# Kernel tuning notes

Hardware: AMD Instinct MI355X
Metric: run time of the kernel (lower is better)

Reference implementation:

```python
import jax, jax.numpy as jnp
import numpy as np

B, T, S, O = 8, 60, 36, 1
H, E, PE = 4, 16, 16
AD, TA, OUT, L = 12, 10, 64, 2
PRUNE_KEEP_FROM = int(np.floor(S * S * 0.5))  # floor(S^2 * (1 - prune_rate))
EPS = 1e-5


def lrelu(v):
    return jax.nn.leaky_relu(v, 0.01)


def pos_encode(times):
    # standard sinusoidal PE on raw timestamps -> (B, T, PE)
    half = PE // 2
    div = jnp.exp(jnp.arange(half, dtype=jnp.float32) * (-jnp.log(10000.0) / half))
    ang = times[..., None] * div
    return jnp.stack([jnp.sin(ang), jnp.cos(ang)], axis=-1).reshape(times.shape + (PE,))


def pair_sim(adj):
    # sum_{i<j} ||a_i - a_j||^2 = B*sum_i||a_i||^2 - ||sum_i a_i||^2
    b = adj.shape[0]
    sq = jnp.sum(adj * adj)
    tot = jnp.sum(adj, axis=0)
    return (b * sq - jnp.sum(tot * tot)) / ((b - 1) ** 2) / (S * S)


def _forward(x, times, mask, bn_g, bn_b, obs_emb_w, attn_w, bidir_w, proj_W, proj_b,
             Wq, bq, Wk, bk, Ws, bs, lnt_g, lnt_b, Wse, bse, lns_g, lns_b):
    b = x.shape[0]
    # BatchNorm2d over timestep channels (training-mode batch stats)
    mu = x.mean(axis=(0, 2, 3), keepdims=True)
    var = x.var(axis=(0, 2, 3), keepdims=True)
    x = (x - mu) / jnp.sqrt(var + EPS) * bn_g[None, :, None, None] + bn_b[None, :, None, None]
    # per-sensor observation embedding: (B,T,S,O) x (S,O,E*H) -> (B,H,T,S,E)
    h = lrelu(jnp.einsum('btso,som->btsm', x, obs_emb_w))
    h = h.reshape(b, T, S, H, E).transpose(0, 3, 1, 2, 4)
    h = h * mask[:, None, :, :, None]
    pe = pos_encode(times)  # (B,T,PE)
    adj = jnp.ones((b, H, S, S), x.dtype)
    sim = pair_sim(adj)  # 0 for all-ones init, kept for faithfulness
    prune_msk = None
    for lay in range(L):
        hp = h @ proj_W.T + proj_b  # (B,H,T,S,AD+PE)
        cat = jnp.concatenate([
            jnp.broadcast_to(attn_w[lay][None, :, None], (b, H, T, S, AD)),
            jnp.broadcast_to(pe[:, None, :, None], (b, H, T, S, PE))], axis=-1)
        alpha = lrelu(jnp.einsum('bhtsd,bhtjd->bhtsj', hp, cat))  # (B,H,T,S,S)
        if lay:
            cnt = mask.sum(axis=1)[:, None, :, None]  # (B,1,S,1)
            adj = lrelu(adj * (alpha.sum(axis=2) / cnt))
            if prune_msk is None:
                flat = adj.reshape(b, H, S * S)
                ranks = jnp.argsort(jnp.argsort(flat, axis=-1), axis=-1)
                prune_msk = (ranks >= PRUNE_KEEP_FROM).astype(adj.dtype).reshape(b, H, S, S)
            adj = adj * prune_msk
            sim = sim + pair_sim(adj)
        bidir = lrelu(jnp.einsum('hsd,hjd->hsj', bidir_w[lay], bidir_w[lay]))  # (H,S,S)
        w = lrelu(bidir[None, :, None] * alpha * adj[:, :, None])  # (B,H,T,S,S)
        # broadcast message passing: (B,H,T,1,S,E) * (B,H,T,S,S,1) -> sum over source sensor
        h = lrelu(jnp.sum(lrelu(h[:, :, :, None, :, :] * w[..., None]), axis=4))
    pe_e = jnp.broadcast_to(pe[:, None, :, None], (b, H, T, S, PE))
    Hc = jnp.concatenate([h, pe_e], axis=-1).transpose(0, 1, 3, 2, 4)  # (B,H,S,T,E+PE)
    Q = Hc @ Wq.T + bq
    K = Hc @ Wk.T + bk
    beta = jnp.einsum('bhstd,bhsud->bhstu', Q, K)  # (B,H,S,T,T)
    beta = (beta @ Ws.T + bs)[..., 0]  # (B,H,S,T)
    m = beta.mean(axis=(-2, -1), keepdims=True)
    v = beta.var(axis=(-2, -1), keepdims=True)
    beta = (beta - m) / jnp.sqrt(v + EPS) * lnt_g + lnt_b
    out = lrelu(jnp.einsum('bhst,bhstd->bhsd', beta, Hc))
    out = lrelu(out @ Wse.T + bse)
    m2 = out.mean(axis=(-2, -1), keepdims=True)
    v2 = out.var(axis=(-2, -1), keepdims=True)
    out = (out - m2) / jnp.sqrt(v2 + EPS) * lns_g + lns_b
    out = out.transpose(0, 2, 1, 3).reshape(b, S, OUT)
    return out, sim


def setup_inputs():
    key = jax.random.key(0)
    ks = jax.random.split(key, 12)
    def rn(k, shape, scale=0.1):
        return jax.random.normal(k, shape, jnp.float32) * scale
    return {
        'x': jax.random.normal(ks[0], (B, T, S, O), jnp.float32),
        'times': jnp.tile(jnp.arange(T, dtype=jnp.float32), (B, 1)),
        'mask': jnp.ones((B, T, S), jnp.float32),
        'bn_g': jnp.ones((T,), jnp.float32),
        'bn_b': jnp.zeros((T,), jnp.float32),
        'obs_emb_w': rn(ks[1], (S, O, E * H)),
        'attn_w': rn(ks[2], (L, H, S, AD)),
        'bidir_w': rn(ks[3], (L, H, S, AD)),
        'proj_W': rn(ks[4], (AD + PE, E)),
        'proj_b': jnp.zeros((AD + PE,), jnp.float32),
        'Wq': rn(ks[5], (TA, E + PE)),
        'bq': jnp.zeros((TA,), jnp.float32),
        'Wk': rn(ks[6], (TA, E + PE)),
        'bk': jnp.zeros((TA,), jnp.float32),
        'Ws': rn(ks[7], (1, T)),
        'bs': jnp.zeros((1,), jnp.float32),
        'lnt_g': jnp.ones((S, T), jnp.float32),
        'lnt_b': jnp.zeros((S, T), jnp.float32),
        'Wse': rn(ks[8], (OUT // H, E + PE)),
        'bse': jnp.zeros((OUT // H,), jnp.float32),
        'lns_g': jnp.ones((S, OUT // H), jnp.float32),
        'lns_b': jnp.zeros((S, OUT // H), jnp.float32),
    }


def reference(x, times, mask, bn_g, bn_b, obs_emb_w, attn_w, bidir_w, proj_W, proj_b,
              Wq, bq, Wk, bk, Ws, bs, lnt_g, lnt_b, Wse, bse, lns_g, lns_b):
    return _forward(x, times, mask, bn_g, bn_b, obs_emb_w, attn_w, bidir_w, proj_W, proj_b,
                    Wq, bq, Wk, bk, Ws, bs, lnt_g, lnt_b, Wse, bse, lns_g, lns_b)
```

## Files before the change

kernel.cpp:

```cpp
#include <hip/hip_runtime.h>
#include <math.h>

#define Bc 8
#define Tc 60
#define Sc 36
#define Hc_ 4
#define Ec 16
#define PEc 16
#define ADc 12
#define TAc 10
#define OUTc 64
#define KEEP 648
#define EPSc 1e-5f
#define LOG1E4_8 1.15129254649702284f

#define WS_H2     18176
#define WS_H1     1124096
#define WS_ALPHA  2230016
#define WS_ADJ    4759808
#define WS_ADJP   4801280
#define WS_CNT    5050112
#define WS_BETA   WS_ALPHA
#define WS_PART   (WS_ALPHA + 69120)
#define WS_OUT2   (WS_ALPHA + 71424)
#define WS_PART2  (WS_ALPHA + 89856)

__device__ __forceinline__ float lrelu(float v){ return v >= 0.f ? v : 0.01f*v; }

__global__ __launch_bounds__(256) void k_layer01(const float* __restrict__ x,
                          const float* __restrict__ times,
                          const float* __restrict__ mask,
                          const float* __restrict__ bn_g,
                          const float* __restrict__ bn_b,
                          const float* __restrict__ obs_w,
                          const float* __restrict__ attn,
                          const float* __restrict__ bidw,
                          const float* __restrict__ projW,
                          const float* __restrict__ projb,
                          float* __restrict__ ws){
    int idx = blockIdx.x;
    int t = idx % Tc; int bh = idx / Tc; int h = bh % Hc_; int b = bh / Hc_;
    int tid = threadIdx.x;
    __shared__ float sh_h[Sc*Ec];
    __shared__ float sh_h1[Sc*Ec];
    __shared__ float sh_pe[PEc];
    __shared__ float sh_at0T[ADc*Sc];
    __shared__ float sh_at1T[ADc*Sc];
    __shared__ float sh_bwT[ADc*Sc];
    __shared__ float sh_hp[Sc*28];
    __shared__ float sh_P[Sc];
    __shared__ float sh_w[Sc*Sc];
    __shared__ float sh_xn[Sc];
    __shared__ float sh_m[Sc];
    __shared__ float sred[8];
    float s0 = 0.f, s1 = 0.f;
    for (int i = tid; i < Bc*Sc; i += 256){
        float v = x[((i/Sc)*Tc + t)*Sc + (i%Sc)];
        s0 += v; s1 += v*v;
    }
    #pragma unroll
    for (int off = 32; off; off >>= 1){
        s0 += __shfl_down(s0, off, 64);
        s1 += __shfl_down(s1, off, 64);
    }
    if ((tid & 63) == 0){ sred[(tid>>6)*2] = s0; sred[(tid>>6)*2 + 1] = s1; }
    if (tid >= 64 && tid < 80){
        int q = tid - 64; int j = q >> 1;
        float ang = times[b*Tc + t] * expf(-(float)j * LOG1E4_8);
        sh_pe[q] = (q & 1) ? cosf(ang) : sinf(ang);
    }
    for (int i = tid; i < ADc*Sc; i += 256){
        int d = i / Sc, j = i % Sc;
        sh_at0T[i] = attn[h*Sc*ADc + j*ADc + d];
        sh_at1T[i] = attn[(Hc_ + h)*Sc*ADc + j*ADc + d];
        sh_bwT[i]  = bidw[h*Sc*ADc + j*ADc + d];
    }
    __syncthreads();
    float mu  = (sred[0]+sred[2]+sred[4]+sred[6]) / (float)(Bc*Sc);
    float var = (sred[1]+sred[3]+sred[5]+sred[7]) / (float)(Bc*Sc) - mu*mu;
    if (tid < Sc){
        float xv = x[(b*Tc + t)*Sc + tid];
        sh_xn[tid] = (xv - mu) * rsqrtf(var + EPSc) * bn_g[t] + bn_b[t];
        sh_m[tid]  = mask[(b*Tc + t)*Sc + tid];
    }
    __syncthreads();
    for (int i = tid; i < Sc*Ec; i += 256){
        int s = i / Ec, e = i % Ec;
        sh_h[i] = lrelu(sh_xn[s]*obs_w[s*64 + h*Ec + e]) * sh_m[s];
    }
    __syncthreads();
    for (int i = tid; i < Sc*28; i += 256){
        int s = i / 28, d = i % 28;
        float acc = projb[d];
        const float* w = projW + d*Ec;
        const float* hh = sh_h + s*Ec;
        #pragma unroll
        for (int e = 0; e < Ec; e++) acc += hh[e]*w[e];
        sh_hp[i] = acc;
    }
    __syncthreads();
    if (tid < Sc){
        const float* hp = sh_hp + tid*28 + ADc;
        float p = 0.f;
        #pragma unroll
        for (int d = 0; d < PEc; d++) p += hp[d]*sh_pe[d];
        sh_P[tid] = p;
    }
    __syncthreads();
    for (int i = tid; i < Sc*Sc; i += 256){
        int s = i / Sc, j = i % Sc;
        const float* hp = sh_hp + s*28;
        float acc = sh_P[s];
        float bd = 0.f;
        #pragma unroll
        for (int d = 0; d < ADc; d++){
            acc += hp[d]*sh_at0T[d*Sc + j];
            bd  += sh_bwT[d*Sc + s]*sh_bwT[d*Sc + j];
        }
        sh_w[i] = lrelu(lrelu(bd)*lrelu(acc));
    }
    __syncthreads();
    float* h1g = ws + WS_H1 + (size_t)idx*Sc*Ec;
    for (int i = tid; i < Sc*Ec; i += 256){
        int s = i / Ec, e = i % Ec;
        float acc = 0.f;
        #pragma unroll 6
        for (int j = 0; j < Sc; j++) acc += lrelu(sh_h[j*Ec + e]*sh_w[s*Sc + j]);
        float v = lrelu(acc);
        sh_h1[i] = v;
        h1g[i] = v;
    }
    __syncthreads();
    for (int i = tid; i < Sc*28; i += 256){
        int s = i / 28, d = i % 28;
        float acc = projb[d];
        const float* w = projW + d*Ec;
        const float* hh = sh_h1 + s*Ec;
        #pragma unroll
        for (int e = 0; e < Ec; e++) acc += hh[e]*w[e];
        sh_hp[i] = acc;
    }
    __syncthreads();
    if (tid < Sc){
        const float* hp = sh_hp + tid*28 + ADc;
        float p = 0.f;
        #pragma unroll
        for (int d = 0; d < PEc; d++) p += hp[d]*sh_pe[d];
        sh_P[tid] = p;
    }
    __syncthreads();
    float* adst = ws + WS_ALPHA + (size_t)idx*Sc*Sc;
    for (int i = tid; i < Sc*Sc; i += 256){
        int s = i / Sc, j = i % Sc;
        const float* hp = sh_hp + s*28;
        float acc = sh_P[s];
        #pragma unroll
        for (int d = 0; d < ADc; d++) acc += hp[d]*sh_at1T[d*Sc + j];
        adst[i] = lrelu(acc);
    }
}

__global__ __launch_bounds__(256) void k_adjpart(const float* __restrict__ mask, float* __restrict__ ws){
    int bh = blockIdx.x / 6; int chunk = blockIdx.x % 6;
    int tid = threadIdx.x;
    const float4* a = (const float4*)(ws + WS_ALPHA + (size_t)bh*Tc*Sc*Sc) + (size_t)chunk*10*324;
    float4* p = (float4*)(ws + WS_ADJP + (size_t)blockIdx.x*Sc*Sc);
    for (int c = tid; c < 324; c += 256){
        float4 acc = make_float4(0.f, 0.f, 0.f, 0.f);
        #pragma unroll
        for (int tt = 0; tt < 10; tt++){
            float4 u = a[(size_t)tt*324 + c];
            acc.x += u.x; acc.y += u.y; acc.z += u.z; acc.w += u.w;
        }
        p[c] = acc;
    }
    if (chunk == 0 && (bh & 3) == 0 && tid < Sc){
        int b = bh >> 2;
        float c = 0.f;
        #pragma unroll 4
        for (int t = 0; t < Tc; t++) c += mask[(b*Tc + t)*Sc + tid];
        ws[WS_CNT + b*Sc + tid] = c;
    }
}

__global__ __launch_bounds__(256) void k_prune(float* __restrict__ ws){
    int bh = blockIdx.x / 24; int chunk = blockIdx.x % 24;
    int b = bh >> 2;
    int tid = threadIdx.x;
    __shared__ __align__(16) float sh_v[Sc*Sc];
    __shared__ float sh_cnt[Sc];
    const float4* p = (const float4*)(ws + WS_ADJP + (size_t)bh*6*Sc*Sc);
    for (int c = tid; c < 324; c += 256){
        float4 acc = make_float4(0.f, 0.f, 0.f, 0.f);
        #pragma unroll
        for (int q = 0; q < 6; q++){
            float4 u = p[(size_t)q*324 + c];
            acc.x += u.x; acc.y += u.y; acc.z += u.z; acc.w += u.w;
        }
        ((float4*)sh_v)[c] = acc;
    }
    if (tid < Sc) sh_cnt[tid] = ws[WS_CNT + b*Sc + tid];
    __syncthreads();
    for (int i = tid; i < Sc*Sc; i += 256){
        int s = i / Sc;
        sh_v[i] = lrelu(sh_v[i] / sh_cnt[s]);
    }
    __syncthreads();
    int r = tid >> 2; if (r > 53) r = 53;
    int part = tid & 3;
    int i = chunk*54 + r;
    float v = sh_v[i];
    const float4* v4 = (const float4*)sh_v + part*81;
    int a0 = part*324;
    int cnt = 0;
    #pragma unroll 9
    for (int j = 0; j < 81; j++){
        float4 u = v4[j];
        int k = a0 + j*4;
        cnt += (int)(u.x < v) + ((int)(u.x == v) & (int)(k   < i));
        cnt += (int)(u.y < v) + ((int)(u.y == v) & (int)(k+1 < i));
        cnt += (int)(u.z < v) + ((int)(u.z == v) & (int)(k+2 < i));
        cnt += (int)(u.w < v) + ((int)(u.w == v) & (int)(k+3 < i));
    }
    cnt += __shfl_down(cnt, 2, 4);
    cnt += __shfl_down(cnt, 1, 4);
    if (part == 0 && tid < 216)
        ws[WS_ADJ + bh*Sc*Sc + i] = (cnt >= KEEP) ? v : 0.f;
}

__global__ __launch_bounds__(256) void k_layer1mp(const float* __restrict__ bidw,
                                                  float* __restrict__ ws){
    int idx = blockIdx.x;
    int bh = idx / Tc; int h = bh % Hc_;
    int tid = threadIdx.x;
    __shared__ float sh_h[Sc*Ec];
    __shared__ float sh_w[Sc*Sc];
    __shared__ float sh_bwT[ADc*Sc];
    const float* hsrc = ws + WS_H1 + (size_t)idx*Sc*Ec;
    float*       hdst = ws + WS_H2 + (size_t)idx*Sc*Ec;
    const float* al  = ws + WS_ALPHA + (size_t)idx*Sc*Sc;
    const float* adj = ws + WS_ADJ + bh*Sc*Sc;
    for (int i = tid; i < Sc*Ec; i += 256) sh_h[i] = hsrc[i];
    for (int i = tid; i < ADc*Sc; i += 256){
        int d = i / Sc, j = i % Sc;
        sh_bwT[i] = bidw[(Hc_ + h)*Sc*ADc + j*ADc + d];
    }
    __syncthreads();
    for (int i = tid; i < Sc*Sc; i += 256){
        int s = i / Sc, j = i % Sc;
        float bd = 0.f;
        #pragma unroll
        for (int d = 0; d < ADc; d++) bd += sh_bwT[d*Sc + s]*sh_bwT[d*Sc + j];
        sh_w[i] = lrelu(lrelu(bd)*al[i]*adj[i]);
    }
    __syncthreads();
    for (int i = tid; i < Sc*Ec; i += 256){
        int s = i / Ec, e = i % Ec;
        float acc = 0.f;
        #pragma unroll 6
        for (int j = 0; j < Sc; j++) acc += lrelu(sh_h[j*Ec + e]*sh_w[s*Sc + j]);
        hdst[i] = lrelu(acc);
    }
}

__global__ __launch_bounds__(64) void kF1(const float* __restrict__ Wq, const float* __restrict__ bq,
                   const float* __restrict__ Wk, const float* __restrict__ bk,
                   const float* __restrict__ Ws_, const float* __restrict__ bs_,
                   const float* __restrict__ times, float* __restrict__ ws){
    int idx = blockIdx.x;
    int s = idx % Sc; int bh = idx / Sc; int b = bh / Hc_;
    int tid = threadIdx.x;
    __shared__ float sh_Hc[Tc*33];
    __shared__ float sh_K[Tc*11];
    __shared__ float sh_Wq[TAc*32];
    __shared__ float sh_WkT[32*TAc];
    __shared__ float sh_bq[TAc], sh_bk[TAc];
    __shared__ float sh_ws[Tc];
    __shared__ float sh_Kw[TAc];
    const float* h2 = ws + WS_H2 + (size_t)bh*Tc*Sc*Ec + s*Ec;
    for (int i4 = tid; i4 < Tc*4; i4 += 64){
        int t = i4 >> 2, c4 = i4 & 3;
        float4 u = *(const float4*)(h2 + t*Sc*Ec + c4*4);
        float* d = sh_Hc + t*33 + c4*4;
        d[0] = u.x; d[1] = u.y; d[2] = u.z; d[3] = u.w;
    }
    for (int i = tid; i < Tc*PEc; i += 64){
        int t = i / PEc, q = i % PEc; int j = q >> 1;
        float ang = times[b*Tc + t] * expf(-(float)j * LOG1E4_8);
        sh_Hc[t*33 + Ec + q] = (q & 1) ? cosf(ang) : sinf(ang);
    }
    for (int i = tid; i < TAc*32; i += 64){
        sh_Wq[i] = Wq[i];
        int d = i / 32, q = i % 32;
        sh_WkT[q*TAc + d] = Wk[i];
    }
    if (tid < TAc){ sh_bq[tid] = bq[tid]; sh_bk[tid] = bk[tid]; }
    if (tid < Tc) sh_ws[tid] = Ws_[tid];
    __syncthreads();
    for (int i = tid; i < Tc*TAc; i += 64){
        int t = i / TAc, d = i % TAc;
        const float* hc = sh_Hc + t*33;
        float acc = sh_bk[d];
        #pragma unroll
        for (int q = 0; q < 32; q++) acc += hc[q]*sh_WkT[q*TAc + d];
        sh_K[t*11 + d] = acc;
    }
    __syncthreads();
    if (tid < TAc){
        float acc = 0.f;
        #pragma unroll 4
        for (int t = 0; t < Tc; t++) acc += sh_K[t*11 + tid]*sh_ws[t];
        sh_Kw[tid] = acc;
    }
    __syncthreads();
    float bv = 0.f;
    float bsv = bs_[0];
    if (tid < Tc){
        const float* hc = sh_Hc + tid*33;
        float acc = bsv;
        #pragma unroll
        for (int d = 0; d < TAc; d++){
            const float* wq = sh_Wq + d*32;
            float qv = sh_bq[d];
            #pragma unroll
            for (int q = 0; q < 32; q++) qv += hc[q]*wq[q];
            acc += qv*sh_Kw[d];
        }
        bv = acc;
        ws[WS_BETA + idx*Tc + tid] = acc;
    }
    float p0 = (tid < Tc) ? bv : 0.f;
    float p1 = p0*bv;
    #pragma unroll
    for (int off = 32; off; off >>= 1){
        p0 += __shfl_down(p0, off, 64);
        p1 += __shfl_down(p1, off, 64);
    }
    if (tid == 0){
        ws[WS_PART + idx*2]     = p0;
        ws[WS_PART + idx*2 + 1] = p1;
    }
}

__global__ __launch_bounds__(64) void kF2(const float* __restrict__ lnt_g, const float* __restrict__ lnt_b,
                   const float* __restrict__ Wse, const float* __restrict__ bse,
                   const float* __restrict__ times, float* __restrict__ ws){
    int idx = blockIdx.x;
    int s = idx % Sc; int bh = idx / Sc; int b = bh / Hc_;
    int tid = threadIdx.x;
    __shared__ float sh_Hc[Tc*33];
    __shared__ float sh_beta[Tc];
    __shared__ float sh_o1[32];
    __shared__ float sh_mi[2];
    float p0 = 0.f, p1 = 0.f;
    if (tid < Sc){
        p0 = ws[WS_PART + (bh*Sc + tid)*2];
        p1 = ws[WS_PART + (bh*Sc + tid)*2 + 1];
    }
    #pragma unroll
    for (int off = 32; off; off >>= 1){
        p0 += __shfl_down(p0, off, 64);
        p1 += __shfl_down(p1, off, 64);
    }
    if (tid == 0){
        float m = p0 / (float)(Sc*Tc);
        sh_mi[0] = m;
        sh_mi[1] = rsqrtf(p1 / (float)(Sc*Tc) - m*m + EPSc);
    }
    const float* h2 = ws + WS_H2 + (size_t)bh*Tc*Sc*Ec + s*Ec;
    for (int i4 = tid; i4 < Tc*4; i4 += 64){
        int t = i4 >> 2, c4 = i4 & 3;
        float4 u = *(const float4*)(h2 + t*Sc*Ec + c4*4);
        float* d = sh_Hc + t*33 + c4*4;
        d[0] = u.x; d[1] = u.y; d[2] = u.z; d[3] = u.w;
    }
    for (int i = tid; i < Tc*PEc; i += 64){
        int t = i / PEc, q = i % PEc; int j = q >> 1;
        float ang = times[b*Tc + t] * expf(-(float)j * LOG1E4_8);
        sh_Hc[t*33 + Ec + q] = (q & 1) ? cosf(ang) : sinf(ang);
    }
    __syncthreads();
    float m = sh_mi[0], inv = sh_mi[1];
    if (tid < Tc){
        float bvv = ws[WS_BETA + idx*Tc + tid];
        sh_beta[tid] = (bvv - m)*inv*lnt_g[s*Tc + tid] + lnt_b[s*Tc + tid];
    }
    __syncthreads();
    if (tid < 32){
        float acc = 0.f;
        #pragma unroll 4
        for (int t = 0; t < Tc; t++) acc += sh_beta[t]*sh_Hc[t*33 + tid];
        sh_o1[tid] = lrelu(acc);
    }
    __syncthreads();
    float v = 0.f;
    if (tid < 16){
        float acc = bse[tid];
        const float* w = Wse + tid*32;
        #pragma unroll
        for (int d = 0; d < 32; d++) acc += sh_o1[d]*w[d];
        v = lrelu(acc);
        ws[WS_OUT2 + idx*16 + tid] = v;
    }
    float q0 = v, q1 = v*v;
    #pragma unroll
    for (int off = 32; off; off >>= 1){
        q0 += __shfl_down(q0, off, 64);
        q1 += __shfl_down(q1, off, 64);
    }
    if (tid == 0){
        ws[WS_PART2 + idx*2]     = q0;
        ws[WS_PART2 + idx*2 + 1] = q1;
    }
}

__global__ __launch_bounds__(256) void kF3s(const float* __restrict__ lns_g, const float* __restrict__ lns_b,
                    const float* __restrict__ ws, float* __restrict__ out){
    int tid = threadIdx.x;
    if (blockIdx.x == 32){
        float sq = 0.f, t2 = 0.f;
        for (int i = tid; i < Hc_*Sc*Sc; i += 256){
            float tot = 0.f;
            #pragma unroll
            for (int b = 0; b < Bc; b++){
                float v = ws[WS_ADJ + b*Hc_*Sc*Sc + i];
                sq += v*v; tot += v;
            }
            t2 += tot*tot;
        }
        __shared__ float r0[256], r1[256];
        r0[tid] = sq; r1[tid] = t2; __syncthreads();
        for (int off = 128; off; off >>= 1){
            if (tid < off){ r0[tid] += r0[tid+off]; r1[tid] += r1[tid+off]; }
            __syncthreads();
        }
        if (tid == 0)
            out[Bc*Sc*OUTc] = ((float)Bc*r0[0] - r1[0]) / 49.f / 1296.f;
        return;
    }
    int bh = blockIdx.x; int h = bh % Hc_; int b = bh / Hc_;
    __shared__ float sh_mi[2];
    if (tid < 64){
        float p0 = 0.f, p1 = 0.f;
        if (tid < Sc){
            p0 = ws[WS_PART2 + (bh*Sc + tid)*2];
            p1 = ws[WS_PART2 + (bh*Sc + tid)*2 + 1];
        }
        #pragma unroll
        for (int off = 32; off; off >>= 1){
            p0 += __shfl_down(p0, off, 64);
            p1 += __shfl_down(p1, off, 64);
        }
        if (tid == 0){
            float m = p0 / (float)(Sc*16);
            sh_mi[0] = m;
            sh_mi[1] = rsqrtf(p1 / (float)(Sc*16) - m*m + EPSc);
        }
    }
    __syncthreads();
    float m2 = sh_mi[0], inv2 = sh_mi[1];
    for (int i = tid; i < Sc*16; i += 256){
        int s = i / 16, k = i % 16;
        float v = ws[WS_OUT2 + bh*Sc*16 + i];
        out[(b*Sc + s)*OUTc + h*16 + k] = (v - m2)*inv2*lns_g[i] + lns_b[i];
    }
}

extern "C" void kernel_launch(void* const* d_in, const int* in_sizes, int n_in,
                              void* d_out, int out_size, void* d_ws, size_t ws_size,
                              hipStream_t stream){
    const float* x     = (const float*)d_in[0];
    const float* times = (const float*)d_in[1];
    const float* mask  = (const float*)d_in[2];
    const float* bn_g  = (const float*)d_in[3];
    const float* bn_b  = (const float*)d_in[4];
    const float* obs   = (const float*)d_in[5];
    const float* attn  = (const float*)d_in[6];
    const float* bidw  = (const float*)d_in[7];
    const float* projW = (const float*)d_in[8];
    const float* projb = (const float*)d_in[9];
    const float* Wq    = (const float*)d_in[10];
    const float* bq    = (const float*)d_in[11];
    const float* Wk    = (const float*)d_in[12];
    const float* bk    = (const float*)d_in[13];
    const float* Ws_   = (const float*)d_in[14];
    const float* bs_   = (const float*)d_in[15];
    const float* lnt_g = (const float*)d_in[16];
    const float* lnt_b = (const float*)d_in[17];
    const float* Wse   = (const float*)d_in[18];
    const float* bse   = (const float*)d_in[19];
    const float* lns_g = (const float*)d_in[20];
    const float* lns_b = (const float*)d_in[21];
    float* ws  = (float*)d_ws;
    float* out = (float*)d_out;

    k_layer01<<<Bc*Hc_*Tc, 256, 0, stream>>>(x, times, mask, bn_g, bn_b, obs, attn, bidw, projW, projb, ws);
    k_adjpart<<<Bc*Hc_*6, 256, 0, stream>>>(mask, ws);
    k_prune<<<Bc*Hc_*24, 256, 0, stream>>>(ws);
    k_layer1mp<<<Bc*Hc_*Tc, 256, 0, stream>>>(bidw, ws);
    kF1<<<Bc*Hc_*Sc, 64, 0, stream>>>(Wq, bq, Wk, bk, Ws_, bs_, times, ws);
    kF2<<<Bc*Hc_*Sc, 64, 0, stream>>>(lnt_g, lnt_b, Wse, bse, times, ws);
    kF3s<<<Bc*Hc_ + 1, 256, 0, stream>>>(lns_g, lns_b, ws, out);
}
```

Before: 209.8 us.

## Precompute bidir weights and positional encodings, fold final layernorm into kF2 via tickets

Computes the layer-1 bidirectional weight matrix and the sinusoidal positional encodings once per (b,h) and per b inside k_adjpart and stores them in workspace, so k_layer1mp, kF1 and kF2 no longer recompute them per block. The adjacency-similarity reduction moves into an extra block of k_layer1mp. The last kF2 block per (b,h), chosen with an atomic ticket counter, applies the final layernorm, which removes the kF3s launch. This trades redundant math and one kernel launch for extra workspace traffic plus threadfence and atomic synchronization.

```diff
diff --git a/kernel.cpp b/kernel.cpp
--- a/kernel.cpp
+++ b/kernel.cpp
@@ -20,6 +20,9 @@
 #define WS_ADJ    4759808
 #define WS_ADJP   4801280
 #define WS_CNT    5050112
+#define WS_BID1   5050400
+#define WS_PET    5091872
+#define WS_TKT    5099552
 #define WS_BETA   WS_ALPHA
 #define WS_PART   (WS_ALPHA + 69120)
 #define WS_OUT2   (WS_ALPHA + 71424)
@@ -160,7 +163,10 @@
     }
 }
 
-__global__ __launch_bounds__(256) void k_adjpart(const float* __restrict__ mask, float* __restrict__ ws){
+__global__ __launch_bounds__(256) void k_adjpart(const float* __restrict__ mask,
+                          const float* __restrict__ bidw,
+                          const float* __restrict__ times,
+                          float* __restrict__ ws){
     int bh = blockIdx.x / 6; int chunk = blockIdx.x % 6;
     int tid = threadIdx.x;
     const float4* a = (const float4*)(ws + WS_ALPHA + (size_t)bh*Tc*Sc*Sc) + (size_t)chunk*10*324;
@@ -180,6 +186,27 @@
         #pragma unroll 4
         for (int t = 0; t < Tc; t++) c += mask[(b*Tc + t)*Sc + tid];
         ws[WS_CNT + b*Sc + tid] = c;
+    }
+    if (blockIdx.x == 0 && tid < 32)
+        ((int*)(ws + WS_TKT))[tid] = 0;
+    if (chunk == 1){
+        int h = bh % Hc_;
+        const float* bw = bidw + (Hc_ + h)*Sc*ADc;
+        for (int i = tid; i < Sc*Sc; i += 256){
+            int s = i / Sc, j = i % Sc;
+            float bd = 0.f;
+            #pragma unroll
+            for (int d = 0; d < ADc; d++) bd += bw[s*ADc + d]*bw[j*ADc + d];
+            ws[WS_BID1 + bh*Sc*Sc + i] = lrelu(bd);
+        }
+    }
+    if (chunk == 2 && (bh & 3) == 0){
+        int b = bh >> 2;
+        for (int i = tid; i < Tc*PEc; i += 256){
+            int t = i / PEc, q = i % PEc; int j = q >> 1;
+            float ang = times[b*Tc + t] * expf(-(float)j * LOG1E4_8);
+            ws[WS_PET + (b*Tc + t)*PEc + q] = (q & 1) ? cosf(ang) : sinf(ang);
+        }
     }
 }
 
@@ -228,31 +255,41 @@
         ws[WS_ADJ + bh*Sc*Sc + i] = (cnt >= KEEP) ? v : 0.f;
 }
 
-__global__ __launch_bounds__(256) void k_layer1mp(const float* __restrict__ bidw,
-                                                  float* __restrict__ ws){
+__global__ __launch_bounds__(256) void k_layer1mp(float* __restrict__ ws, float* __restrict__ out){
+    int tid = threadIdx.x;
+    if (blockIdx.x == Bc*Hc_*Tc){
+        float sq = 0.f, t2 = 0.f;
+        for (int i = tid; i < Hc_*Sc*Sc; i += 256){
+            float tot = 0.f;
+            #pragma unroll
+            for (int b = 0; b < Bc; b++){
+                float v = ws[WS_ADJ + b*Hc_*Sc*Sc + i];
+                sq += v*v; tot += v;
+            }
+            t2 += tot*tot;
+        }
+        __shared__ float r0[256], r1[256];
+        r0[tid] = sq; r1[tid] = t2; __syncthreads();
+        for (int off = 128; off; off >>= 1){
+            if (tid < off){ r0[tid] += r0[tid+off]; r1[tid] += r1[tid+off]; }
+            __syncthreads();
+        }
+        if (tid == 0)
+            out[Bc*Sc*OUTc] = ((float)Bc*r0[0] - r1[0]) / 49.f / 1296.f;
+        return;
+    }
     int idx = blockIdx.x;
-    int bh = idx / Tc; int h = bh % Hc_;
-    int tid = threadIdx.x;
+    int bh = idx / Tc;
     __shared__ float sh_h[Sc*Ec];
     __shared__ float sh_w[Sc*Sc];
-    __shared__ float sh_bwT[ADc*Sc];
     const float* hsrc = ws + WS_H1 + (size_t)idx*Sc*Ec;
     float*       hdst = ws + WS_H2 + (size_t)idx*Sc*Ec;
     const float* al  = ws + WS_ALPHA + (size_t)idx*Sc*Sc;
     const float* adj = ws + WS_ADJ + bh*Sc*Sc;
+    const float* bid = ws + WS_BID1 + bh*Sc*Sc;
     for (int i = tid; i < Sc*Ec; i += 256) sh_h[i] = hsrc[i];
-    for (int i = tid; i < ADc*Sc; i += 256){
-        int d = i / Sc, j = i % Sc;
-        sh_bwT[i] = bidw[(Hc_ + h)*Sc*ADc + j*ADc + d];
-    }
-    __syncthreads();
-    for (int i = tid; i < Sc*Sc; i += 256){
-        int s = i / Sc, j = i % Sc;
-        float bd = 0.f;
-        #pragma unroll
-        for (int d = 0; d < ADc; d++) bd += sh_bwT[d*Sc + s]*sh_bwT[d*Sc + j];
-        sh_w[i] = lrelu(lrelu(bd)*al[i]*adj[i]);
-    }
+    for (int i = tid; i < Sc*Sc; i += 256)
+        sh_w[i] = lrelu(bid[i]*al[i]*adj[i]);
     __syncthreads();
     for (int i = tid; i < Sc*Ec; i += 256){
         int s = i / Ec, e = i % Ec;
@@ -266,7 +303,7 @@
 __global__ __launch_bounds__(64) void kF1(const float* __restrict__ Wq, const float* __restrict__ bq,
                    const float* __restrict__ Wk, const float* __restrict__ bk,
                    const float* __restrict__ Ws_, const float* __restrict__ bs_,
-                   const float* __restrict__ times, float* __restrict__ ws){
+                   float* __restrict__ ws){
     int idx = blockIdx.x;
     int s = idx % Sc; int bh = idx / Sc; int b = bh / Hc_;
     int tid = threadIdx.x;
@@ -284,11 +321,9 @@
         float* d = sh_Hc + t*33 + c4*4;
         d[0] = u.x; d[1] = u.y; d[2] = u.z; d[3] = u.w;
     }
-    for (int i = tid; i < Tc*PEc; i += 64){
-        int t = i / PEc, q = i % PEc; int j = q >> 1;
-        float ang = times[b*Tc + t] * expf(-(float)j * LOG1E4_8);
-        sh_Hc[t*33 + Ec + q] = (q & 1) ? cosf(ang) : sinf(ang);
-    }
+    const float* pet = ws + WS_PET + b*Tc*PEc;
+    for (int i = tid; i < Tc*PEc; i += 64)
+        sh_Hc[(i/PEc)*33 + Ec + (i%PEc)] = pet[i];
     for (int i = tid; i < TAc*32; i += 64){
         sh_Wq[i] = Wq[i];
         int d = i / 32, q = i % 32;
@@ -344,14 +379,16 @@
 
 __global__ __launch_bounds__(64) void kF2(const float* __restrict__ lnt_g, const float* __restrict__ lnt_b,
                    const float* __restrict__ Wse, const float* __restrict__ bse,
-                   const float* __restrict__ times, float* __restrict__ ws){
+                   const float* __restrict__ lns_g, const float* __restrict__ lns_b,
+                   float* __restrict__ ws, float* __restrict__ out){
     int idx = blockIdx.x;
-    int s = idx % Sc; int bh = idx / Sc; int b = bh / Hc_;
+    int s = idx % Sc; int bh = idx / Sc; int b = bh / Hc_; int h = bh % Hc_;
     int tid = threadIdx.x;
     __shared__ float sh_Hc[Tc*33];
     __shared__ float sh_beta[Tc];
     __shared__ float sh_o1[32];
     __shared__ float sh_mi[2];
+    __shared__ int sh_last;
     float p0 = 0.f, p1 = 0.f;
     if (tid < Sc){
         p0 = ws[WS_PART + (bh*Sc + tid)*2];
@@ -374,11 +411,9 @@
         float* d = sh_Hc + t*33 + c4*4;
         d[0] = u.x; d[1] = u.y; d[2] = u.z; d[3] = u.w;
     }
-    for (int i = tid; i < Tc*PEc; i += 64){
-        int t = i / PEc, q = i % PEc; int j = q >> 1;
-        float ang = times[b*Tc + t] * expf(-(float)j * LOG1E4_8);
-        sh_Hc[t*33 + Ec + q] = (q & 1) ? cosf(ang) : sinf(ang);
-    }
+    const float* pet = ws + WS_PET + b*Tc*PEc;
+    for (int i = tid; i < Tc*PEc; i += 64)
+        sh_Hc[(i/PEc)*33 + Ec + (i%PEc)] = pet[i];
     __syncthreads();
     float m = sh_mi[0], inv = sh_mi[1];
     if (tid < Tc){
@@ -412,57 +447,35 @@
         ws[WS_PART2 + idx*2]     = q0;
         ws[WS_PART2 + idx*2 + 1] = q1;
     }
-}
-
-__global__ __launch_bounds__(256) void kF3s(const float* __restrict__ lns_g, const float* __restrict__ lns_b,
-                    const float* __restrict__ ws, float* __restrict__ out){
-    int tid = threadIdx.x;
-    if (blockIdx.x == 32){
-        float sq = 0.f, t2 = 0.f;
-        for (int i = tid; i < Hc_*Sc*Sc; i += 256){
-            float tot = 0.f;
-            #pragma unroll
-            for (int b = 0; b < Bc; b++){
-                float v = ws[WS_ADJ + b*Hc_*Sc*Sc + i];
-                sq += v*v; tot += v;
-            }
-            t2 += tot*tot;
-        }
-        __shared__ float r0[256], r1[256];
-        r0[tid] = sq; r1[tid] = t2; __syncthreads();
-        for (int off = 128; off; off >>= 1){
-            if (tid < off){ r0[tid] += r0[tid+off]; r1[tid] += r1[tid+off]; }
-            __syncthreads();
-        }
-        if (tid == 0)
-            out[Bc*Sc*OUTc] = ((float)Bc*r0[0] - r1[0]) / 49.f / 1296.f;
-        return;
-    }
-    int bh = blockIdx.x; int h = bh % Hc_; int b = bh / Hc_;
-    __shared__ float sh_mi[2];
-    if (tid < 64){
-        float p0 = 0.f, p1 = 0.f;
-        if (tid < Sc){
-            p0 = ws[WS_PART2 + (bh*Sc + tid)*2];
-            p1 = ws[WS_PART2 + (bh*Sc + tid)*2 + 1];
-        }
-        #pragma unroll
-        for (int off = 32; off; off >>= 1){
-            p0 += __shfl_down(p0, off, 64);
-            p1 += __shfl_down(p1, off, 64);
-        }
-        if (tid == 0){
-            float m = p0 / (float)(Sc*16);
-            sh_mi[0] = m;
-            sh_mi[1] = rsqrtf(p1 / (float)(Sc*16) - m*m + EPSc);
-        }
+    __threadfence();
+    if (tid == 0){
+        int old = atomicAdd((int*)(ws + WS_TKT) + bh, 1);
+        sh_last = (old == Sc - 1);
+    }
+    __syncthreads();
+    if (!sh_last) return;
+    __threadfence();
+    float r0 = 0.f, r1 = 0.f;
+    if (tid < Sc){
+        r0 = ws[WS_PART2 + (bh*Sc + tid)*2];
+        r1 = ws[WS_PART2 + (bh*Sc + tid)*2 + 1];
+    }
+    #pragma unroll
+    for (int off = 32; off; off >>= 1){
+        r0 += __shfl_down(r0, off, 64);
+        r1 += __shfl_down(r1, off, 64);
+    }
+    if (tid == 0){
+        float m2 = r0 / (float)(Sc*16);
+        sh_mi[0] = m2;
+        sh_mi[1] = rsqrtf(r1 / (float)(Sc*16) - m2*m2 + EPSc);
     }
     __syncthreads();
     float m2 = sh_mi[0], inv2 = sh_mi[1];
-    for (int i = tid; i < Sc*16; i += 256){
-        int s = i / 16, k = i % 16;
-        float v = ws[WS_OUT2 + bh*Sc*16 + i];
-        out[(b*Sc + s)*OUTc + h*16 + k] = (v - m2)*inv2*lns_g[i] + lns_b[i];
+    for (int i = tid; i < Sc*16; i += 64){
+        int ss = i / 16, k = i % 16;
+        float vv = ws[WS_OUT2 + bh*Sc*16 + i];
+        out[(b*Sc + ss)*OUTc + h*16 + k] = (vv - m2)*inv2*lns_g[i] + lns_b[i];
     }
 }
 
@@ -495,10 +508,9 @@
     float* out = (float*)d_out;
 
     k_layer01<<<Bc*Hc_*Tc, 256, 0, stream>>>(x, times, mask, bn_g, bn_b, obs, attn, bidw, projW, projb, ws);
-    k_adjpart<<<Bc*Hc_*6, 256, 0, stream>>>(mask, ws);
+    k_adjpart<<<Bc*Hc_*6, 256, 0, stream>>>(mask, bidw, times, ws);
     k_prune<<<Bc*Hc_*24, 256, 0, stream>>>(ws);
-    k_layer1mp<<<Bc*Hc_*Tc, 256, 0, stream>>>(bidw, ws);
-    kF1<<<Bc*Hc_*Sc, 64, 0, stream>>>(Wq, bq, Wk, bk, Ws_, bs_, times, ws);
-    kF2<<<Bc*Hc_*Sc, 64, 0, stream>>>(lnt_g, lnt_b, Wse, bse, times, ws);
-    kF3s<<<Bc*Hc_ + 1, 256, 0, stream>>>(lns_g, lns_b, ws, out);
-}
+    k_layer1mp<<<Bc*Hc_*Tc + 1, 256, 0, stream>>>(ws, out);
+    kF1<<<Bc*Hc_*Sc, 64, 0, stream>>>(Wq, bq, Wk, bk, Ws_, bs_, ws);
+    kF2<<<Bc*Hc_*Sc, 64, 0, stream>>>(lnt_g, lnt_b, Wse, bse, lns_g, lns_b, ws, out);
+}
```

Result: slower. 236.0 us (+12.5%).
